# Kernel optimization log

Hardware: AMD Instinct MI355X
Metric: run time of the kernel (lower is better)

The kernel has to match this reference:

```python
import jax, jax.numpy as jnp
import numpy as np

N_NODES = 65536
N_GRAPHS = 64


def gcn_conv(x, W, b, src, dst, n):
    # PyG GCNConv: add self-loops, symmetric normalization D^-1/2 (A+I) D^-1/2, then linear.
    xw = x @ W  # [N, F_out]
    deg = jnp.zeros((n,), x.dtype).at[dst].add(1.0) + 1.0  # +1 for self-loop
    dinv = jax.lax.rsqrt(deg)
    norm = dinv[src] * dinv[dst]  # [E]
    agg = jnp.zeros_like(xw).at[dst].add(xw[src] * norm[:, None])
    agg = agg + xw * (dinv * dinv)[:, None]  # self-loop term, norm_ii = 1/deg_i
    return agg + b


def setup_inputs() -> dict:
    key = jax.random.key(0)
    ks = jax.random.split(key, 8)
    E = 524288
    x = jax.random.normal(ks[0], (N_NODES, 1), jnp.float32)
    edge_index = jax.random.randint(ks[1], (2, E), 0, N_NODES, dtype=jnp.int64)
    batch = jnp.sort(jax.random.randint(ks[2], (N_NODES,), 0, N_GRAPHS, dtype=jnp.int64))
    def glorot(k, fi, fo):
        s = np.sqrt(2.0 / (fi + fo)).astype(np.float32)
        return jax.random.normal(k, (fi, fo), jnp.float32) * s
    return {
        "x": x, "edge_index": edge_index, "batch": batch,
        "W1": glorot(ks[3], 1, 128), "b1": jnp.zeros((128,), jnp.float32),
        "W2": glorot(ks[4], 128, 64), "b2": jnp.zeros((64,), jnp.float32),
        "W3": glorot(ks[5], 64, 32), "b3": jnp.zeros((32,), jnp.float32),
        "Wfc": glorot(ks[6], 32, 10), "bfc": jnp.zeros((10,), jnp.float32),
    }


def reference(x, edge_index, batch, W1, b1, W2, b2, W3, b3, Wfc, bfc):
    src, dst = edge_index[0], edge_index[1]
    n = x.shape[0]
    h = jax.nn.relu(gcn_conv(x, W1, b1, src, dst, n))
    # dropout is identity in eval mode
    h = jax.nn.relu(gcn_conv(h, W2, b2, src, dst, n))
    h = jax.nn.relu(gcn_conv(h, W3, b3, src, dst, n))
    # global mean pool per graph
    sums = jax.ops.segment_sum(h, batch, num_segments=N_GRAPHS)  # [B, 32]
    cnts = jax.ops.segment_sum(jnp.ones((n,), h.dtype), batch, num_segments=N_GRAPHS)
    pooled = sums / jnp.maximum(cnts, 1.0)[:, None]
    return pooled @ Wfc + bfc  # [B, 10]
```

## Files before the change

kernel.cpp:

```cpp
#include <hip/hip_runtime.h>
#include <hip/hip_fp16.h>

#define THREADS 256
#define CAP 64

typedef union { uint2 u; __half2 h[2]; } H4;
typedef union { uint4 u; __half2 h[4]; } H8;

__global__ void k_build(const int* __restrict__ src, const int* __restrict__ dst,
                        int* __restrict__ counts, int* __restrict__ esrc, int E) {
    int e = blockIdx.x * blockDim.x + threadIdx.x;
    if (e >= E) return;
    int d = dst[e];
    int s = atomicAdd(&counts[d], 1);
    if (s < CAP) esrc[d * CAP + s] = src[e];
}

__global__ void k_prep(const int* __restrict__ counts, const float* __restrict__ x,
                       float* __restrict__ dinv, float* __restrict__ s1, int N) {
    int i = blockIdx.x * blockDim.x + threadIdx.x;
    if (i >= N) return;
    float d = rsqrtf((float)counts[i] + 1.0f);
    dinv[i] = d;
    s1[i] = x[i] * d;
}

#define L12_R 8
__global__ void k_l1l2(const float* __restrict__ s1, const float* __restrict__ dinv,
                       const int* __restrict__ counts, const int* __restrict__ esrc,
                       const float* __restrict__ W1, const float* __restrict__ b1,
                       const float* __restrict__ W2, __half* __restrict__ xws2, int N) {
    __shared__ float wb[128 * 2];
    __shared__ float W2s[128 * 64];
    __shared__ float als[128];
    __shared__ float dls[128];
    for (int idx = threadIdx.x; idx < 128; idx += 256) {
        wb[idx * 2] = W1[idx];
        wb[idx * 2 + 1] = b1[idx];
    }
    for (int idx = threadIdx.x; idx < 128 * 64 / 4; idx += 256)
        reinterpret_cast<float4*>(W2s)[idx] = reinterpret_cast<const float4*>(W2)[idx];
    if (threadIdx.x < 128) {
        int i = blockIdx.x * 128 + threadIdx.x;
        float a = 0.f, di = 0.f;
        if (i < N) {
            di = dinv[i];
            float t = s1[i];
            int q = i * CAP, end = q + min(counts[i], CAP);
            for (; q + 7 < end; q += 8) {
                int a0 = esrc[q], a1 = esrc[q + 1], a2 = esrc[q + 2], a3 = esrc[q + 3];
                int a4 = esrc[q + 4], a5 = esrc[q + 5], a6 = esrc[q + 6], a7 = esrc[q + 7];
                float v0 = s1[a0], v1 = s1[a1], v2 = s1[a2], v3 = s1[a3];
                float v4 = s1[a4], v5 = s1[a5], v6 = s1[a6], v7 = s1[a7];
                t += ((v0 + v1) + (v2 + v3)) + ((v4 + v5) + (v6 + v7));
            }
            for (; q + 3 < end; q += 4) {
                int a0 = esrc[q], a1 = esrc[q + 1], a2 = esrc[q + 2], a3 = esrc[q + 3];
                float v0 = s1[a0], v1 = s1[a1], v2 = s1[a2], v3 = s1[a3];
                t += (v0 + v1) + (v2 + v3);
            }
            for (; q < end; ++q) t += s1[esrc[q]];
            a = di * t;
        }
        als[threadIdx.x] = a;
        dls[threadIdx.x] = di;
    }
    __syncthreads();

    int c4 = threadIdx.x & 15;
    int rg = threadIdx.x >> 4;
    int base = blockIdx.x * 128 + rg * L12_R;

    float a[L12_R];
#pragma unroll
    for (int r = 0; r < L12_R; ++r) a[r] = als[rg * L12_R + r];

    float4 acc[L12_R] = {};
    for (int k = 0; k < 128; ++k) {
        float2 w1b1 = *reinterpret_cast<const float2*>(&wb[k * 2]);
        float4 w2 = *reinterpret_cast<const float4*>(&W2s[k * 64 + c4 * 4]);
#pragma unroll
        for (int r = 0; r < L12_R; ++r) {
            float h = fmaxf(fmaf(a[r], w1b1.x, w1b1.y), 0.f);
            acc[r].x = fmaf(h, w2.x, acc[r].x);
            acc[r].y = fmaf(h, w2.y, acc[r].y);
            acc[r].z = fmaf(h, w2.z, acc[r].z);
            acc[r].w = fmaf(h, w2.w, acc[r].w);
        }
    }
#pragma unroll
    for (int r = 0; r < L12_R; ++r) {
        int i = base + r;
        if (i < N) {
            float di = dls[rg * L12_R + r];
            H4 o;
            o.h[0] = __floats2half2_rn(acc[r].x * di, acc[r].y * di);
            o.h[1] = __floats2half2_rn(acc[r].z * di, acc[r].w * di);
            reinterpret_cast<uint2*>(xws2)[(size_t)i * 16 + c4] = o.u;
        }
    }
}

__global__ void k_l2l3(const int* __restrict__ counts, const int* __restrict__ esrc,
                       const __half* __restrict__ xws2, const float* __restrict__ dinv,
                       const float* __restrict__ b2, const float* __restrict__ W3,
                       __half* __restrict__ xws3, int N) {
    __shared__ float W3s[64 * 32];
    __shared__ float h2s[32][68];
    __shared__ float b2s[64];
    for (int idx = threadIdx.x; idx < 64 * 32 / 4; idx += 256)
        reinterpret_cast<float4*>(W3s)[idx] = reinterpret_cast<const float4*>(W3)[idx];
    if (threadIdx.x < 64) b2s[threadIdx.x] = b2[threadIdx.x];
    __syncthreads();

    {
        int c8 = threadIdx.x & 7;
        int r  = threadIdx.x >> 3;
        int i  = blockIdx.x * 32 + r;
        if (i < N) {
            const uint4* x4 = reinterpret_cast<const uint4*>(xws2);
            H8 p; p.u = x4[(size_t)i * 8 + c8];
            float acc[8];
#pragma unroll
            for (int j = 0; j < 4; ++j) {
                float2 f = __half22float2(p.h[j]);
                acc[2 * j] = f.x; acc[2 * j + 1] = f.y;
            }
            int q = i * CAP, end = q + min(counts[i], CAP);
            for (; q + 3 < end; q += 4) {
                int sa = esrc[q], sb = esrc[q + 1], sc = esrc[q + 2], sd = esrc[q + 3];
                H8 pa, pb, pc, pd;
                pa.u = x4[(size_t)sa * 8 + c8];
                pb.u = x4[(size_t)sb * 8 + c8];
                pc.u = x4[(size_t)sc * 8 + c8];
                pd.u = x4[(size_t)sd * 8 + c8];
#pragma unroll
                for (int j = 0; j < 4; ++j) {
                    float2 fa = __half22float2(pa.h[j]);
                    float2 fb = __half22float2(pb.h[j]);
                    float2 fc = __half22float2(pc.h[j]);
                    float2 fd = __half22float2(pd.h[j]);
                    acc[2 * j]     += (fa.x + fb.x) + (fc.x + fd.x);
                    acc[2 * j + 1] += (fa.y + fb.y) + (fc.y + fd.y);
                }
            }
            for (; q < end; ++q) {
                H8 pe; pe.u = x4[(size_t)esrc[q] * 8 + c8];
#pragma unroll
                for (int j = 0; j < 4; ++j) {
                    float2 f = __half22float2(pe.h[j]);
                    acc[2 * j] += f.x; acc[2 * j + 1] += f.y;
                }
            }
            float di = dinv[i];
            float hv[8];
#pragma unroll
            for (int j = 0; j < 8; ++j)
                hv[j] = fmaxf(fmaf(di, acc[j], b2s[c8 * 8 + j]), 0.f);
            float4 hv0 = {hv[0], hv[1], hv[2], hv[3]};
            float4 hv1 = {hv[4], hv[5], hv[6], hv[7]};
            *reinterpret_cast<float4*>(&h2s[r][c8 * 8])     = hv0;
            *reinterpret_cast<float4*>(&h2s[r][c8 * 8 + 4]) = hv1;
        }
    }
    __syncthreads();
    {
        int c  = threadIdx.x & 7;
        int r2 = threadIdx.x >> 3;
        int i2 = blockIdx.x * 32 + r2;
        if (i2 >= N) return;
        float4 acc = {};
#pragma unroll
        for (int k = 0; k < 64; ++k) {
            float h = h2s[r2][k];
            float4 w = *reinterpret_cast<const float4*>(&W3s[k * 32 + c * 4]);
            acc.x = fmaf(h, w.x, acc.x);
            acc.y = fmaf(h, w.y, acc.y);
            acc.z = fmaf(h, w.z, acc.z);
            acc.w = fmaf(h, w.w, acc.w);
        }
        float di = dinv[i2];
        H4 o;
        o.h[0] = __floats2half2_rn(acc.x * di, acc.y * di);
        o.h[1] = __floats2half2_rn(acc.z * di, acc.w * di);
        reinterpret_cast<uint2*>(xws3)[(size_t)i2 * 8 + c] = o.u;
    }
}

__global__ void k_l3pool(const int* __restrict__ counts, const int* __restrict__ esrc,
                         const __half* __restrict__ xws3, const float* __restrict__ dinv,
                         const float* __restrict__ b3, const int* __restrict__ batch,
                         float* __restrict__ sums, float* __restrict__ cnt,
                         int* __restrict__ ticket, const float* __restrict__ Wfc,
                         const float* __restrict__ bfc, float* __restrict__ out,
                         int N, int nblocks) {
    __shared__ float sl[64 * 32];
    __shared__ float cl[64];
    __shared__ int lastflag;
    for (int idx = threadIdx.x; idx < 64 * 32; idx += 256) sl[idx] = 0.f;
    if (threadIdx.x < 64) cl[threadIdx.x] = 0.f;
    __syncthreads();

    int c = threadIdx.x & 3;
    int r = threadIdx.x >> 2;
    int i = blockIdx.x * 64 + r;
    if (i < N) {
        const uint4* x4 = reinterpret_cast<const uint4*>(xws3);
        H8 p; p.u = x4[(size_t)i * 4 + c];
        float acc[8];
#pragma unroll
        for (int j = 0; j < 4; ++j) {
            float2 f = __half22float2(p.h[j]);
            acc[2 * j] = f.x; acc[2 * j + 1] = f.y;
        }
        int q = i * CAP, end = q + min(counts[i], CAP);
        for (; q + 3 < end; q += 4) {
            int sa = esrc[q], sb = esrc[q + 1], sc = esrc[q + 2], sd = esrc[q + 3];
            H8 pa, pb, pc, pd;
            pa.u = x4[(size_t)sa * 4 + c];
            pb.u = x4[(size_t)sb * 4 + c];
            pc.u = x4[(size_t)sc * 4 + c];
            pd.u = x4[(size_t)sd * 4 + c];
#pragma unroll
            for (int j = 0; j < 4; ++j) {
                float2 fa = __half22float2(pa.h[j]);
                float2 fb = __half22float2(pb.h[j]);
                float2 fc = __half22float2(pc.h[j]);
                float2 fd = __half22float2(pd.h[j]);
                acc[2 * j]     += (fa.x + fb.x) + (fc.x + fd.x);
                acc[2 * j + 1] += (fa.y + fb.y) + (fc.y + fd.y);
            }
        }
        for (; q < end; ++q) {
            H8 pe; pe.u = x4[(size_t)esrc[q] * 4 + c];
#pragma unroll
            for (int j = 0; j < 4; ++j) {
                float2 f = __half22float2(pe.h[j]);
                acc[2 * j] += f.x; acc[2 * j + 1] += f.y;
            }
        }
        float di = dinv[i];
        int g = batch[i];
#pragma unroll
        for (int j = 0; j < 8; ++j)
            atomicAdd(&sl[g * 32 + c * 8 + j], fmaxf(fmaf(di, acc[j], b3[c * 8 + j]), 0.f));
        if (c == 0) atomicAdd(&cl[g], 1.f);
    }
    __syncthreads();

    int start = blockIdx.x * 64;
    if (start < N) {
        int g0 = batch[start];
        int g1 = batch[min(start + 63, N - 1)];
        int ng = g1 - g0 + 1;
        for (int idx = threadIdx.x; idx < ng * 32; idx += 256) {
            float v = sl[(g0 + idx / 32) * 32 + (idx & 31)];
            if (v != 0.f) atomicAdd(&sums[(g0 + idx / 32) * 32 + (idx & 31)], v);
        }
        for (int idx = threadIdx.x; idx < ng; idx += 256) {
            float v = cl[g0 + idx];
            if (v != 0.f) atomicAdd(&cnt[g0 + idx], v);
        }
    }

    asm volatile("s_waitcnt vmcnt(0)" ::: "memory");
    __syncthreads();
    if (threadIdx.x == 0) lastflag = (atomicAdd(ticket, 1) == nblocks - 1) ? 1 : 0;
    __syncthreads();
    if (!lastflag) return;

    for (int idx = threadIdx.x; idx < 64 * 32; idx += 256)
        sl[idx] = __hip_atomic_load(&sums[idx], __ATOMIC_RELAXED, __HIP_MEMORY_SCOPE_AGENT);
    for (int idx = threadIdx.x; idx < 64; idx += 256)
        cl[idx] = __hip_atomic_load(&cnt[idx], __ATOMIC_RELAXED, __HIP_MEMORY_SCOPE_AGENT);
    __syncthreads();
    for (int tix = threadIdx.x; tix < 640; tix += 256) {
        int g = tix / 10, o = tix % 10;
        float inv = 1.0f / fmaxf(cl[g], 1.0f);
        float acc = bfc[o];
#pragma unroll
        for (int f = 0; f < 32; ++f) acc = fmaf(sl[g * 32 + f] * inv, Wfc[f * 10 + o], acc);
        out[tix] = acc;
    }
}

extern "C" void kernel_launch(void* const* d_in, const int* in_sizes, int n_in,
                              void* d_out, int out_size, void* d_ws, size_t ws_size,
                              hipStream_t stream) {
    const float* x    = (const float*)d_in[0];
    const int*   ei   = (const int*)d_in[1];
    const int*   batch= (const int*)d_in[2];
    const float* W1   = (const float*)d_in[3];
    const float* b1   = (const float*)d_in[4];
    const float* W2   = (const float*)d_in[5];
    const float* b2   = (const float*)d_in[6];
    const float* W3   = (const float*)d_in[7];
    const float* b3   = (const float*)d_in[8];
    const float* Wfc  = (const float*)d_in[9];
    const float* bfc  = (const float*)d_in[10];
    float* out = (float*)d_out;

    const int N = in_sizes[0];
    const int E = in_sizes[1] / 2;
    const int* src  = ei;
    const int* dstp = ei + E;

    char* ws = (char*)d_ws;
    size_t off = 0;
    auto alloc = [&](size_t bytes) { void* p = ws + off; off = (off + bytes + 15) & ~(size_t)15; return p; };
    int*    counts   = (int*)   alloc((size_t)N * 4);
    float*  sums     = (float*) alloc(64 * 32 * 4);
    float*  cnt      = (float*) alloc(64 * 4);
    int*    ticket   = (int*)   alloc(16);
    size_t  zbytes   = (size_t)((char*)ticket + 16 - (char*)counts);
    int*    esrc     = (int*)   alloc((size_t)N * CAP * 4);
    float*  dinv     = (float*) alloc((size_t)N * 4);
    float*  s1       = (float*) alloc((size_t)N * 4);
    __half* xws2     = (__half*)alloc((size_t)N * 64 * 2);
    __half* xws3     = (__half*)alloc((size_t)N * 32 * 2);

    auto blocks = [](long n) { return (int)((n + THREADS - 1) / THREADS); };

    hipMemsetAsync(counts, 0, zbytes, stream);

    k_build<<<blocks(E), THREADS, 0, stream>>>(src, dstp, counts, esrc, E);
    k_prep <<<blocks(N), THREADS, 0, stream>>>(counts, x, dinv, s1, N);
    k_l1l2 <<<(N + 127) / 128, THREADS, 0, stream>>>(s1, dinv, counts, esrc,
                                                     W1, b1, W2, xws2, N);
    k_l2l3 <<<(N + 31) / 32, THREADS, 0, stream>>>(counts, esrc, xws2, dinv, b2, W3, xws3, N);
    int npool = (N + 63) / 64;
    k_l3pool<<<npool, THREADS, 0, stream>>>(counts, esrc, xws3, dinv, b3, batch,
                                            sums, cnt, ticket, Wfc, bfc, out, N, npool);
}
```

Measured before the change: 182.3 us.

## Replace layer-2 feature gather with piecewise-linear ReLU breakpoint tables

Layer 1 has one input feature, so relu(a*W1+b1)@W2 is piecewise linear in the scalar a with breakpoints at -b1/w1. The new code sorts the breakpoints, precomputes per-segment slope and intercept tables (SA, SB), and stores one float4 per node (scaled aggregate, dinv, segment index). Layer-2 aggregation then gathers 16 bytes per neighbour instead of a 128-byte half row and rebuilds the features from tables held in LDS. This removes the dense layer-1/2 matmul and most of the gather traffic, but adds per-edge FMA work, LDS table reads and fp16 rounding of the cumulative tables. Keeping the first-layer aggregation bit-identical to the reference also matters, because the segment index is chosen from it.

```diff
diff --git a/kernel.cpp b/kernel.cpp
--- a/kernel.cpp
+++ b/kernel.cpp
@@ -17,97 +17,120 @@
 }
 
 __global__ void k_prep(const int* __restrict__ counts, const float* __restrict__ x,
-                       float* __restrict__ dinv, float* __restrict__ s1, int N) {
-    int i = blockIdx.x * blockDim.x + threadIdx.x;
-    if (i >= N) return;
-    float d = rsqrtf((float)counts[i] + 1.0f);
-    dinv[i] = d;
-    s1[i] = x[i] * d;
-}
-
-#define L12_R 8
-__global__ void k_l1l2(const float* __restrict__ s1, const float* __restrict__ dinv,
-                       const int* __restrict__ counts, const int* __restrict__ esrc,
                        const float* __restrict__ W1, const float* __restrict__ b1,
-                       const float* __restrict__ W2, __half* __restrict__ xws2, int N) {
-    __shared__ float wb[128 * 2];
+                       const float* __restrict__ W2,
+                       float* __restrict__ dinv, float* __restrict__ s1,
+                       float* __restrict__ tsg, __half* __restrict__ SAh,
+                       __half* __restrict__ SBh, int N) {
+    int nprep = (N + 255) / 256;
+    if ((int)blockIdx.x < nprep) {
+        int i = blockIdx.x * 256 + threadIdx.x;
+        if (i < N) {
+            float d = rsqrtf((float)counts[i] + 1.0f);
+            dinv[i] = d;
+            s1[i] = x[i] * d;
+        }
+        return;
+    }
     __shared__ float W2s[128 * 64];
-    __shared__ float als[128];
-    __shared__ float dls[128];
-    for (int idx = threadIdx.x; idx < 128; idx += 256) {
-        wb[idx * 2] = W1[idx];
-        wb[idx * 2 + 1] = b1[idx];
-    }
+    __shared__ float w1s[128], b1s[128], tval[128], ts[128];
+    __shared__ int widx[128];
     for (int idx = threadIdx.x; idx < 128 * 64 / 4; idx += 256)
         reinterpret_cast<float4*>(W2s)[idx] = reinterpret_cast<const float4*>(W2)[idx];
     if (threadIdx.x < 128) {
-        int i = blockIdx.x * 128 + threadIdx.x;
-        float a = 0.f, di = 0.f;
-        if (i < N) {
-            di = dinv[i];
-            float t = s1[i];
-            int q = i * CAP, end = q + min(counts[i], CAP);
-            for (; q + 7 < end; q += 8) {
-                int a0 = esrc[q], a1 = esrc[q + 1], a2 = esrc[q + 2], a3 = esrc[q + 3];
-                int a4 = esrc[q + 4], a5 = esrc[q + 5], a6 = esrc[q + 6], a7 = esrc[q + 7];
-                float v0 = s1[a0], v1 = s1[a1], v2 = s1[a2], v3 = s1[a3];
-                float v4 = s1[a4], v5 = s1[a5], v6 = s1[a6], v7 = s1[a7];
-                t += ((v0 + v1) + (v2 + v3)) + ((v4 + v5) + (v6 + v7));
-            }
-            for (; q + 3 < end; q += 4) {
-                int a0 = esrc[q], a1 = esrc[q + 1], a2 = esrc[q + 2], a3 = esrc[q + 3];
-                float v0 = s1[a0], v1 = s1[a1], v2 = s1[a2], v3 = s1[a3];
-                t += (v0 + v1) + (v2 + v3);
-            }
-            for (; q < end; ++q) t += s1[esrc[q]];
-            a = di * t;
-        }
-        als[threadIdx.x] = a;
-        dls[threadIdx.x] = di;
-    }
-    __syncthreads();
-
-    int c4 = threadIdx.x & 15;
-    int rg = threadIdx.x >> 4;
-    int base = blockIdx.x * 128 + rg * L12_R;
-
-    float a[L12_R];
-#pragma unroll
-    for (int r = 0; r < L12_R; ++r) a[r] = als[rg * L12_R + r];
-
-    float4 acc[L12_R] = {};
-    for (int k = 0; k < 128; ++k) {
-        float2 w1b1 = *reinterpret_cast<const float2*>(&wb[k * 2]);
-        float4 w2 = *reinterpret_cast<const float4*>(&W2s[k * 64 + c4 * 4]);
-#pragma unroll
-        for (int r = 0; r < L12_R; ++r) {
-            float h = fmaxf(fmaf(a[r], w1b1.x, w1b1.y), 0.f);
-            acc[r].x = fmaf(h, w2.x, acc[r].x);
-            acc[r].y = fmaf(h, w2.y, acc[r].y);
-            acc[r].z = fmaf(h, w2.z, acc[r].z);
-            acc[r].w = fmaf(h, w2.w, acc[r].w);
-        }
-    }
-#pragma unroll
-    for (int r = 0; r < L12_R; ++r) {
-        int i = base + r;
-        if (i < N) {
-            float di = dls[rg * L12_R + r];
-            H4 o;
-            o.h[0] = __floats2half2_rn(acc[r].x * di, acc[r].y * di);
-            o.h[1] = __floats2half2_rn(acc[r].z * di, acc[r].w * di);
-            reinterpret_cast<uint2*>(xws2)[(size_t)i * 16 + c4] = o.u;
-        }
-    }
+        float w = W1[threadIdx.x];
+        float b = b1[threadIdx.x];
+        w1s[threadIdx.x] = w;
+        b1s[threadIdx.x] = b;
+        tval[threadIdx.x] = (w != 0.f) ? (-b / w) : __builtin_inff();
+    }
+    __syncthreads();
+    if (threadIdx.x < 128) {
+        float t = tval[threadIdx.x];
+        int r = 0;
+        for (int j = 0; j < 128; ++j) {
+            float tj = tval[j];
+            r += (tj < t || (tj == t && j < (int)threadIdx.x)) ? 1 : 0;
+        }
+        ts[r] = t;
+        widx[r] = threadIdx.x;
+    }
+    __syncthreads();
+    if (threadIdx.x < 128) tsg[threadIdx.x] = ts[threadIdx.x];
+    if (threadIdx.x < 64) {
+        int c = threadIdx.x;
+        float negA = 0.f, negB = 0.f, constB = 0.f;
+        for (int r = 0; r < 128; ++r) {
+            int k = widx[r];
+            float w = w1s[k], b = b1s[k], w2 = W2s[k * 64 + c];
+            if (w < 0.f) { negA += w * w2; negB += b * w2; }
+            else if (w == 0.f && b > 0.f) constB += b * w2;
+        }
+        float posA = 0.f, posB = 0.f, nA = 0.f, nB = 0.f;
+        SAh[c] = __float2half(negA);
+        SBh[c] = __float2half(negB + constB);
+        for (int r = 0; r < 128; ++r) {
+            int k = widx[r];
+            float w = w1s[k], b = b1s[k], w2 = W2s[k * 64 + c];
+            if (w > 0.f) { posA += w * w2; posB += b * w2; }
+            else if (w < 0.f) { nA += w * w2; nB += b * w2; }
+            SAh[(r + 1) * 64 + c] = __float2half(posA + (negA - nA));
+            SBh[(r + 1) * 64 + c] = __float2half(posB + (negB - nB) + constB);
+        }
+    }
+}
+
+__global__ void k_agg1(const float* __restrict__ s1, const float* __restrict__ dinv,
+                       const int* __restrict__ counts, const int* __restrict__ esrc,
+                       const float* __restrict__ tsg, float4* __restrict__ pk, int N) {
+    __shared__ float tsl[128];
+    if (threadIdx.x < 128) tsl[threadIdx.x] = tsg[threadIdx.x];
+    __syncthreads();
+    int i = blockIdx.x * blockDim.x + threadIdx.x;
+    if (i >= N) return;
+    float di = dinv[i];
+    float t = s1[i];
+    int q = i * CAP, end = q + min(counts[i], CAP);
+    for (; q + 7 < end; q += 8) {
+        int a0 = esrc[q], a1 = esrc[q + 1], a2 = esrc[q + 2], a3 = esrc[q + 3];
+        int a4 = esrc[q + 4], a5 = esrc[q + 5], a6 = esrc[q + 6], a7 = esrc[q + 7];
+        float v0 = s1[a0], v1 = s1[a1], v2 = s1[a2], v3 = s1[a3];
+        float v4 = s1[a4], v5 = s1[a5], v6 = s1[a6], v7 = s1[a7];
+        t += ((v0 + v1) + (v2 + v3)) + ((v4 + v5) + (v6 + v7));
+    }
+    for (; q + 3 < end; q += 4) {
+        int a0 = esrc[q], a1 = esrc[q + 1], a2 = esrc[q + 2], a3 = esrc[q + 3];
+        float v0 = s1[a0], v1 = s1[a1], v2 = s1[a2], v3 = s1[a3];
+        t += (v0 + v1) + (v2 + v3);
+    }
+    for (; q < end; ++q) t += s1[esrc[q]];
+    float a = di * t;
+    int lo = 0, hi = 128;
+#pragma unroll
+    for (int it = 0; it < 7; ++it) {
+        int m = (lo + hi) >> 1;
+        if (tsl[m] <= a) lo = m + 1; else hi = m;
+    }
+    pk[i] = make_float4(a * di, di, __int_as_float(lo), 0.f);
 }
 
 __global__ void k_l2l3(const int* __restrict__ counts, const int* __restrict__ esrc,
-                       const __half* __restrict__ xws2, const float* __restrict__ dinv,
-                       const float* __restrict__ b2, const float* __restrict__ W3,
-                       __half* __restrict__ xws3, int N) {
+                       const float4* __restrict__ pk, const float* __restrict__ b2,
+                       const float* __restrict__ W3, const __half* __restrict__ SAh,
+                       const __half* __restrict__ SBh, __half* __restrict__ xws3, int N) {
+    __shared__ __half2 SAs[129 * 32];
+    __shared__ __half2 SBs[129 * 32];
     __shared__ float W3s[64 * 32];
     __shared__ float h2s[32][68];
     __shared__ float b2s[64];
+    {
+        const __half2* sag = reinterpret_cast<const __half2*>(SAh);
+        const __half2* sbg = reinterpret_cast<const __half2*>(SBh);
+        for (int idx = threadIdx.x; idx < 129 * 32; idx += 256) {
+            SAs[idx] = sag[idx];
+            SBs[idx] = sbg[idx];
+        }
+    }
     for (int idx = threadIdx.x; idx < 64 * 32 / 4; idx += 256)
         reinterpret_cast<float4*>(W3s)[idx] = reinterpret_cast<const float4*>(W3)[idx];
     if (threadIdx.x < 64) b2s[threadIdx.x] = b2[threadIdx.x];
@@ -118,49 +141,35 @@
         int r  = threadIdx.x >> 3;
         int i  = blockIdx.x * 32 + r;
         if (i < N) {
-            const uint4* x4 = reinterpret_cast<const uint4*>(xws2);
-            H8 p; p.u = x4[(size_t)i * 8 + c8];
-            float acc[8];
-#pragma unroll
-            for (int j = 0; j < 4; ++j) {
-                float2 f = __half22float2(p.h[j]);
-                acc[2 * j] = f.x; acc[2 * j + 1] = f.y;
-            }
+            float acc[8] = {};
+            auto expand = [&](float4 pv) {
+                int p = __float_as_int(pv.z);
+                const __half2* sa = &SAs[p * 32 + c8 * 4];
+                const __half2* sb = &SBs[p * 32 + c8 * 4];
+#pragma unroll
+                for (int j = 0; j < 4; ++j) {
+                    float2 fa = __half22float2(sa[j]);
+                    float2 fb = __half22float2(sb[j]);
+                    acc[2 * j]     = fmaf(pv.x, fa.x, fmaf(pv.y, fb.x, acc[2 * j]));
+                    acc[2 * j + 1] = fmaf(pv.x, fa.y, fmaf(pv.y, fb.y, acc[2 * j + 1]));
+                }
+            };
+            float4 self = pk[i];
+            float diN = self.y;
+            expand(self);
             int q = i * CAP, end = q + min(counts[i], CAP);
             for (; q + 3 < end; q += 4) {
-                int sa = esrc[q], sb = esrc[q + 1], sc = esrc[q + 2], sd = esrc[q + 3];
-                H8 pa, pb, pc, pd;
-                pa.u = x4[(size_t)sa * 8 + c8];
-                pb.u = x4[(size_t)sb * 8 + c8];
-                pc.u = x4[(size_t)sc * 8 + c8];
-                pd.u = x4[(size_t)sd * 8 + c8];
-#pragma unroll
-                for (int j = 0; j < 4; ++j) {
-                    float2 fa = __half22float2(pa.h[j]);
-                    float2 fb = __half22float2(pb.h[j]);
-                    float2 fc = __half22float2(pc.h[j]);
-                    float2 fd = __half22float2(pd.h[j]);
-                    acc[2 * j]     += (fa.x + fb.x) + (fc.x + fd.x);
-                    acc[2 * j + 1] += (fa.y + fb.y) + (fc.y + fd.y);
-                }
+                int ea = esrc[q], eb = esrc[q + 1], ec = esrc[q + 2], ed = esrc[q + 3];
+                float4 pa = pk[ea], pb = pk[eb], pc = pk[ec], pd = pk[ed];
+                expand(pa); expand(pb); expand(pc); expand(pd);
             }
-            for (; q < end; ++q) {
-                H8 pe; pe.u = x4[(size_t)esrc[q] * 8 + c8];
-#pragma unroll
-                for (int j = 0; j < 4; ++j) {
-                    float2 f = __half22float2(pe.h[j]);
-                    acc[2 * j] += f.x; acc[2 * j + 1] += f.y;
-                }
-            }
-            float di = dinv[i];
+            for (; q < end; ++q) expand(pk[esrc[q]]);
             float hv[8];
 #pragma unroll
             for (int j = 0; j < 8; ++j)
-                hv[j] = fmaxf(fmaf(di, acc[j], b2s[c8 * 8 + j]), 0.f);
-            float4 hv0 = {hv[0], hv[1], hv[2], hv[3]};
-            float4 hv1 = {hv[4], hv[5], hv[6], hv[7]};
-            *reinterpret_cast<float4*>(&h2s[r][c8 * 8])     = hv0;
-            *reinterpret_cast<float4*>(&h2s[r][c8 * 8 + 4]) = hv1;
+                hv[j] = fmaxf(fmaf(diN, acc[j], b2s[c8 * 8 + j]), 0.f);
+            *reinterpret_cast<float4*>(&h2s[r][c8 * 8])     = make_float4(hv[0], hv[1], hv[2], hv[3]);
+            *reinterpret_cast<float4*>(&h2s[r][c8 * 8 + 4]) = make_float4(hv[4], hv[5], hv[6], hv[7]);
         }
     }
     __syncthreads();
@@ -179,7 +188,8 @@
             acc.z = fmaf(h, w.z, acc.z);
             acc.w = fmaf(h, w.w, acc.w);
         }
-        float di = dinv[i2];
+        float4 self2 = pk[i2];
+        float di = self2.y;
         H4 o;
         o.h[0] = __floats2half2_rn(acc.x * di, acc.y * di);
         o.h[1] = __floats2half2_rn(acc.z * di, acc.w * di);
@@ -316,7 +326,10 @@
     int*    esrc     = (int*)   alloc((size_t)N * CAP * 4);
     float*  dinv     = (float*) alloc((size_t)N * 4);
     float*  s1       = (float*) alloc((size_t)N * 4);
-    __half* xws2     = (__half*)alloc((size_t)N * 64 * 2);
+    float*  tsg      = (float*) alloc(128 * 4);
+    __half* SAh      = (__half*)alloc(129 * 64 * 2);
+    __half* SBh      = (__half*)alloc(129 * 64 * 2);
+    float4* pk       = (float4*)alloc((size_t)N * 16);
     __half* xws3     = (__half*)alloc((size_t)N * 32 * 2);
 
     auto blocks = [](long n) { return (int)((n + THREADS - 1) / THREADS); };
@@ -324,10 +337,11 @@
     hipMemsetAsync(counts, 0, zbytes, stream);
 
     k_build<<<blocks(E), THREADS, 0, stream>>>(src, dstp, counts, esrc, E);
-    k_prep <<<blocks(N), THREADS, 0, stream>>>(counts, x, dinv, s1, N);
-    k_l1l2 <<<(N + 127) / 128, THREADS, 0, stream>>>(s1, dinv, counts, esrc,
-                                                     W1, b1, W2, xws2, N);
-    k_l2l3 <<<(N + 31) / 32, THREADS, 0, stream>>>(counts, esrc, xws2, dinv, b2, W3, xws3, N);
+    k_prep <<<(N + 255) / 256 + 1, THREADS, 0, stream>>>(counts, x, W1, b1, W2,
+                                                         dinv, s1, tsg, SAh, SBh, N);
+    k_agg1 <<<blocks(N), THREADS, 0, stream>>>(s1, dinv, counts, esrc, tsg, pk, N);
+    k_l2l3 <<<(N + 31) / 32, THREADS, 0, stream>>>(counts, esrc, pk, b2, W3,
+                                                   SAh, SBh, xws3, N);
     int npool = (N + 63) / 64;
     k_l3pool<<<npool, THREADS, 0, stream>>>(counts, esrc, xws3, dinv, b3, batch,
                                             sums, cnt, ticket, Wfc, bfc, out, N, npool);
```

Result: slower. 200.4 us (+10.0%).
